# Performance work log

Hardware: AMD Instinct MI355X
Metric: run time of the kernel (lower is better)

## Reference

```python
import jax, jax.numpy as jnp
import numpy as np

IMG = 640.0  # square input image, strides 16/32 -> 40x40 and 20x20 grids

def _decode_level(raw, stride):
    # raw: [B, 5+C, H, W] -> [B, H*W, 5+C] with xy/wh decoded (get_output_and_grid)
    b, ch, h, w = raw.shape
    out = raw.transpose(0, 2, 3, 1).reshape(b, h * w, ch)
    yv, xv = jnp.meshgrid(jnp.arange(h), jnp.arange(w), indexing='ij')
    gx = xv.reshape(-1).astype(raw.dtype)
    gy = yv.reshape(-1).astype(raw.dtype)
    xy = (out[..., :2] + jnp.stack([gx, gy], -1)[None]) * stride
    wh = jnp.exp(out[..., 2:4]) * stride
    out = jnp.concatenate([xy, wh, out[..., 4:]], -1)
    return out, gx, gy, jnp.full((h * w,), stride, raw.dtype)

def _pairwise_iou(a, b):
    # a:[M,4], b:[A,4] in cxcywh -> [M,A] (bboxes_iou, xyxy=False)
    tl = jnp.maximum(a[:, None, :2] - a[:, None, 2:] * 0.5, b[None, :, :2] - b[None, :, 2:] * 0.5)
    br = jnp.minimum(a[:, None, :2] + a[:, None, 2:] * 0.5, b[None, :, :2] + b[None, :, 2:] * 0.5)
    inter = jnp.prod(br - tl, -1) * (tl < br).all(-1)
    area_a = a[:, 2] * a[:, 3]
    area_b = b[:, 2] * b[:, 3]
    return inter / (area_a[:, None] + area_b[None, :] - inter + 1e-16)

def _iou_loss(p, t):
    # YOLOX IOUloss (loss_type='iou'): 1 - iou^2, elementwise over [..., 4] cxcywh
    tl = jnp.maximum(p[..., :2] - p[..., 2:] * 0.5, t[..., :2] - t[..., 2:] * 0.5)
    br = jnp.minimum(p[..., :2] + p[..., 2:] * 0.5, t[..., :2] + t[..., 2:] * 0.5)
    inter = jnp.prod(br - tl, -1) * (tl < br).all(-1)
    iou = inter / (p[..., 2] * p[..., 3] + t[..., 2] * t[..., 3] - inter + 1e-16)
    return 1.0 - iou ** 2

def _bce_logits(x, t):
    # BCEWithLogitsLoss(reduction='none') = softplus(x) - x*t (stable)
    return jnp.logaddexp(0.0, x) - x * t

def _assign_one(bbox_p, cls_p, obj_p, gtb, gtc, gtv, ax, ay, st):
    # SimOTA assignment for one image (mask form of get_assignments, which is @no_grad).
    # bbox_p:[A,4] cls_p:[A,C] obj_p:[A] gtb:[M,4] px cxcywh, gtv:[M] valid mask.
    m = gtb.shape[0]
    axc = (ax + 0.5) * st
    ayc = (ay + 0.5) * st
    gl = gtb[:, 0] - 0.5 * gtb[:, 2]; gr = gtb[:, 0] + 0.5 * gtb[:, 2]
    gtp = gtb[:, 1] - 0.5 * gtb[:, 3]; gbt = gtb[:, 1] + 0.5 * gtb[:, 3]
    in_box = ((axc[None] > gl[:, None]) & (axc[None] < gr[:, None]) &
              (ayc[None] > gtp[:, None]) & (ayc[None] < gbt[:, None])) & gtv[:, None]
    r = 2.5  # center_radius
    in_ctr = ((axc[None] > gtb[:, 0:1] - r * st[None]) & (axc[None] < gtb[:, 0:1] + r * st[None]) &
              (ayc[None] > gtb[:, 1:2] - r * st[None]) & (ayc[None] < gtb[:, 1:2] + r * st[None])) & gtv[:, None]
    fg_cand = (in_box | in_ctr).any(0)          # candidate anchors (fg_mask pre-filter)
    in_both = in_box & in_ctr
    ious = _pairwise_iou(gtb, bbox_p)            # [M,A]
    p = jnp.sqrt(jax.nn.sigmoid(cls_p) * jax.nn.sigmoid(obj_p)[:, None])[None]  # [1,A,C]
    t = jax.nn.one_hot(gtc, cls_p.shape[-1], dtype=p.dtype)[:, None, :]          # [M,1,C]
    eps = 1e-12
    cls_cost = -(t * jnp.log(p + eps) + (1.0 - t) * jnp.log(1.0 - p + eps)).sum(-1)
    invalid = (~fg_cand)[None] | (~gtv)[:, None]
    cost = cls_cost - 3.0 * jnp.log(ious + 1e-8) + 1e5 * (~in_both) + 1e9 * invalid
    ious_m = jnp.where(invalid, 0.0, ious)
    topk, _ = jax.lax.top_k(ious_m, 10)
    dk = jnp.maximum(topk.sum(-1).astype(jnp.int32), 1)  # dynamic_k, clamp min=1
    dk = jnp.where(gtv, dk, 0)
    ranks = jnp.argsort(jnp.argsort(cost, axis=1), axis=1)
    matching = ranks < dk[:, None]                        # top dynamic_k lowest-cost anchors per gt
    conflict = matching.sum(0) > 1
    best_gt = jnp.argmin(cost, 0)
    matching = jnp.where(conflict[None], jnp.arange(m)[:, None] == best_gt[None], matching)
    fg = matching.any(0)
    matched = jnp.argmax(matching, 0).astype(jnp.int32)
    pred_iou = jnp.where(matching, ious, 0.0).sum(0)
    return fg, matched, pred_iou

def _forward(out_l0, out_l1, gt_boxes, gt_classes, num_gts):
    ncls = out_l0.shape[1] - 5
    decs, xs, ys, ss = [], [], [], []
    for raw, stride in ((out_l0, 16.0), (out_l1, 32.0)):
        d, gx, gy, s = _decode_level(raw, stride)
        decs.append(d); xs.append(gx); ys.append(gy); ss.append(s)
    outputs = jnp.concatenate(decs, 1)  # [B, A, 5+C]
    ax = jnp.concatenate(xs); ay = jnp.concatenate(ys); st = jnp.concatenate(ss)
    bbox_p = outputs[..., :4]; obj_p = outputs[..., 4]; cls_p = outputs[..., 5:]
    gtb = gt_boxes * IMG  # normalized -> pixels (imgs_w == imgs_h == IMG)
    gtv = jnp.arange(gt_boxes.shape[1])[None, :] < num_gts[:, None]
    sg = jax.lax.stop_gradient  # get_assignments runs under torch.no_grad
    fg, matched, pred_iou = jax.vmap(_assign_one, in_axes=(0, 0, 0, 0, 0, 0, None, None, None))(
        sg(bbox_p), sg(cls_p), sg(obj_p), sg(gtb), gt_classes, gtv, ax, ay, st)
    fgf = fg.astype(outputs.dtype)
    cls_t = jax.nn.one_hot(jnp.take_along_axis(gt_classes, matched, 1), ncls,
                           dtype=outputs.dtype) * pred_iou[..., None] * fgf[..., None]
    reg_t = jnp.take_along_axis(gtb, matched[..., None], 1)  # [B,A,4]
    num_fg = jnp.maximum(fgf.sum(), 1.0)
    loss_iou = (_iou_loss(bbox_p, reg_t) * fgf).sum() / num_fg
    loss_obj = _bce_logits(obj_p, fgf).sum() / num_fg
    loss_cls = (_bce_logits(cls_p, cls_t) * fgf[..., None]).sum() / num_fg
    total = 5.0 * loss_iou + loss_obj + loss_cls
    return (total, 5.0 * loss_iou, loss_obj, loss_cls,
            num_fg / jnp.maximum(num_gts.sum().astype(outputs.dtype), 1.0))

def setup_inputs() -> dict:
    key = jax.random.key(0)
    k1, k2, k3, k4, k5 = jax.random.split(key, 5)
    return {
        'out_l0': jax.random.normal(k1, (64, 25, 40, 40), jnp.float32),
        'out_l1': jax.random.normal(k2, (64, 25, 20, 20), jnp.float32),
        'gt_boxes': jax.random.uniform(k3, (64, 100, 4), jnp.float32, 1e-3, 1.0),
        'gt_classes': jax.random.randint(k4, (64, 100), 0, 20).astype(jnp.int32),
        'num_gts': jax.random.randint(k5, (64,), 0, 100).astype(jnp.int32),
    }

def reference(out_l0, out_l1, gt_boxes, gt_classes, num_gts):
    return _forward(out_l0, out_l1, gt_boxes, gt_classes, num_gts)
```

## Files before the change

### kernel.cpp

```cpp
#include <hip/hip_runtime.h>
#include <cfloat>
#include <climits>

#define NB 64
#define NA 2000
#define NAP 2048
#define NA0 1600
#define NC 20
#define NM 100

__device__ __forceinline__ void anchor_geom(int a, float& axc, float& ayc, float& st) {
    if (a < NA0) {
        st = 16.0f;
        int x = a % 40, y = a / 40;
        axc = ((float)x + 0.5f) * 16.0f;
        ayc = ((float)y + 0.5f) * 16.0f;
    } else {
        st = 32.0f;
        int aa = a - NA0;
        int x = aa % 20, y = aa / 20;
        axc = ((float)x + 0.5f) * 32.0f;
        ayc = ((float)y + 0.5f) * 32.0f;
    }
}

__device__ __forceinline__ float cost_pair(const float4 g, float clsc, const float4 pb,
                                           float axc, float ayc, float st, bool fc) {
    float tlx = fmaxf(g.x - 0.5f * g.z, pb.x - 0.5f * pb.z);
    float tly = fmaxf(g.y - 0.5f * g.w, pb.y - 0.5f * pb.w);
    float brx = fminf(g.x + 0.5f * g.z, pb.x + 0.5f * pb.z);
    float bry = fminf(g.y + 0.5f * g.w, pb.y + 0.5f * pb.w);
    float inter = (brx - tlx) * (bry - tly);
    bool ok = (tlx < brx) && (tly < bry);
    inter = ok ? inter : 0.0f;
    float iou = inter / ((g.z * g.w + pb.z * pb.w) - inter + 1e-16f);
    bool ib = (axc > g.x - 0.5f * g.z) && (axc < g.x + 0.5f * g.z)
           && (ayc > g.y - 0.5f * g.w) && (ayc < g.y + 0.5f * g.w);
    bool ic = (axc > g.x - 2.5f * st) && (axc < g.x + 2.5f * st)
           && (ayc > g.y - 2.5f * st) && (ayc < g.y + 2.5f * st);
    return ((clsc - 3.0f * __logf(iou + 1e-8f)) + ((ib && ic) ? 0.0f : 1e5f)) + (fc ? 0.0f : 1e9f);
}

__device__ __forceinline__ unsigned int wave_max_u32(unsigned int x) {
    unsigned int y;
    y = (unsigned)__builtin_amdgcn_update_dpp((int)x, (int)x, 0x111, 0xf, 0xf, false); x = max(x, y);
    y = (unsigned)__builtin_amdgcn_update_dpp((int)x, (int)x, 0x112, 0xf, 0xf, false); x = max(x, y);
    y = (unsigned)__builtin_amdgcn_update_dpp((int)x, (int)x, 0x114, 0xf, 0xf, false); x = max(x, y);
    y = (unsigned)__builtin_amdgcn_update_dpp((int)x, (int)x, 0x118, 0xf, 0xf, false); x = max(x, y);
    y = (unsigned)__builtin_amdgcn_update_dpp((int)x, (int)x, 0x142, 0xa, 0xf, false); x = max(x, y);
    y = (unsigned)__builtin_amdgcn_update_dpp((int)x, (int)x, 0x143, 0xc, 0xf, false); x = max(x, y);
    return (unsigned)__builtin_amdgcn_readlane((int)x, 63);
}
__device__ __forceinline__ unsigned int wave_min_u32(unsigned int x) {
    unsigned int y;
    y = (unsigned)__builtin_amdgcn_update_dpp((int)x, (int)x, 0x111, 0xf, 0xf, false); x = min(x, y);
    y = (unsigned)__builtin_amdgcn_update_dpp((int)x, (int)x, 0x112, 0xf, 0xf, false); x = min(x, y);
    y = (unsigned)__builtin_amdgcn_update_dpp((int)x, (int)x, 0x114, 0xf, 0xf, false); x = min(x, y);
    y = (unsigned)__builtin_amdgcn_update_dpp((int)x, (int)x, 0x118, 0xf, 0xf, false); x = min(x, y);
    y = (unsigned)__builtin_amdgcn_update_dpp((int)x, (int)x, 0x142, 0xa, 0xf, false); x = min(x, y);
    y = (unsigned)__builtin_amdgcn_update_dpp((int)x, (int)x, 0x143, 0xc, 0xf, false); x = min(x, y);
    return (unsigned)__builtin_amdgcn_readlane((int)x, 63);
}

__global__ __launch_bounds__(256) void k_decode(const float* __restrict__ l0, const float* __restrict__ l1,
                                                const float* __restrict__ gt_boxes, const int* __restrict__ num_gts,
                                                float4* __restrict__ dec, float* __restrict__ qq,
                                                unsigned long long* __restrict__ fgw, unsigned int* __restrict__ cm,
                                                float* __restrict__ sp) {
    int b = blockIdx.y;
    int a = blockIdx.x * 256 + threadIdx.x;
    int lane = threadIdx.x & 63;
    __shared__ float4 sext[NM];
    __shared__ float2 sctr[NM];
    __shared__ int sng;
    if (threadIdx.x < NM) {
        float4 g = ((const float4*)gt_boxes)[b * NM + threadIdx.x];
        g.x *= 640.0f; g.y *= 640.0f; g.z *= 640.0f; g.w *= 640.0f;
        sext[threadIdx.x] = make_float4(g.x - 0.5f * g.z, g.x + 0.5f * g.z,
                                        g.y - 0.5f * g.w, g.y + 0.5f * g.w);
        sctr[threadIdx.x] = make_float2(g.x, g.y);
    }
    if (threadIdx.x == 0) sng = num_gts[b];
    __syncthreads();

    bool real = a < NA;
    size_t pidx = (size_t)b * NAP + a;

    if (!real) {
        dec[pidx] = make_float4(0.f, 0.f, 0.f, 0.f);
#pragma unroll
        for (int c = 0; c < NC; c++) qq[((size_t)b * NC + c) * NAP + a] = 0.0f;
        cm[pidx] = 0;
        sp[pidx] = 0.0f;
        unsigned long long mk = __ballot(0);
        if (lane == 0) fgw[(size_t)b * 32 + (a >> 6)] = mk;
        return;
    }

    float v[25];
    if (a < NA0) {
        const float* p = l0 + (size_t)b * 25 * NA0 + a;
#pragma unroll
        for (int c = 0; c < 25; c++) v[c] = p[(size_t)c * NA0];
    } else {
        const float* p = l1 + (size_t)b * 25 * 400 + (a - NA0);
#pragma unroll
        for (int c = 0; c < 25; c++) v[c] = p[(size_t)c * 400];
    }
    float axc, ayc, st;
    anchor_geom(a, axc, ayc, st);
    float gx, gy;
    if (a < NA0) { gx = (float)(a % 40); gy = (float)(a / 40); }
    else { int aa = a - NA0; gx = (float)(aa % 20); gy = (float)(aa / 20); }
    float4 pb;
    pb.x = (v[0] + gx) * st;
    pb.y = (v[1] + gy) * st;
    pb.z = expf(v[2]) * st;
    pb.w = expf(v[3]) * st;
    dec[pidx] = pb;

    float sob = 1.0f / (1.0f + __expf(-v[4]));
    float d[NC];
    float s = 0.0f;
    float spv = 0.0f;
#pragma unroll
    for (int c = 0; c < NC; c++) {
        float x = v[5 + c];
        float sc = 1.0f / (1.0f + __expf(-x));
        float p = sqrtf(sc * sob);
        float lp = __logf(p + 1e-12f);
        float lq = __logf(1.0f - p + 1e-12f);
        s += -lq;
        d[c] = lq - lp;
        spv += fmaxf(x, 0.0f) + log1pf(__expf(-fabsf(x)));
    }
#pragma unroll
    for (int c = 0; c < NC; c++)
        qq[((size_t)b * NC + c) * NAP + a] = s + d[c];
    sp[pidx] = spv;

    int ng = sng;
    int f = 0;
    float rst = 2.5f * st;
    for (int m = 0; m < ng; m++) {
        float4 e = sext[m];
        float2 cc = sctr[m];
        bool ib = (axc > e.x) && (axc < e.y) && (ayc > e.z) && (ayc < e.w);
        bool ic = (axc > cc.x - rst) && (axc < cc.x + rst) && (ayc > cc.y - rst) && (ayc < cc.y + rst);
        if (ib || ic) { f = 1; break; }
    }
    unsigned long long mk = __ballot(f);
    if (lane == 0) fgw[(size_t)b * 32 + (a >> 6)] = mk;
    cm[pidx] = 0;
}

__global__ __launch_bounds__(256) void k_assign(const float* __restrict__ gt_boxes, const int* __restrict__ gt_classes,
                                                const int* __restrict__ num_gts, const float4* __restrict__ dec,
                                                const float* __restrict__ qq, const unsigned long long* __restrict__ fgw,
                                                unsigned int* __restrict__ cm) {
    int lane = threadIdx.x & 63;
    int wv = __builtin_amdgcn_readfirstlane((int)(threadIdx.x >> 6));
    int rloc = wv >> 1, half = wv & 1;
    int row = __builtin_amdgcn_readfirstlane((int)(blockIdx.x * 2 + rloc));
    int b = row / NM, m = row - b * NM;
    bool valid = (m < num_gts[b]);

    __shared__ unsigned int lA[2][2][10];
    __shared__ unsigned int lB[2][2][10];
    __shared__ unsigned int lmeta[2];
    __shared__ unsigned int lthr[2];

    unsigned int ik[16], ck[16];
    size_t bNA = (size_t)b * NAP;
    unsigned int inc = (1u << 20) + (unsigned)m;

    if (valid) {
        float4 g = ((const float4*)gt_boxes)[b * NM + m];
        g.x *= 640.0f; g.y *= 640.0f; g.z *= 640.0f; g.w *= 640.0f;
        int tc = gt_classes[b * NM + m];
        const float* qrow = qq + ((size_t)b * NC + tc) * NAP;

        float glx = g.x - 0.5f * g.z, grx = g.x + 0.5f * g.z;
        float gty = g.y - 0.5f * g.w, gby = g.y + 0.5f * g.w;
        float areag = g.z * g.w;
        float c16l = g.x - 40.0f, c16r = g.x + 40.0f, c16t = g.y - 40.0f, c16b = g.y + 40.0f;
        float c32l = g.x - 80.0f, c32r = g.x + 80.0f, c32t = g.y - 80.0f, c32b = g.y + 80.0f;

#pragma unroll
        for (int j = 0; j < 16; j++) {
            int jj = half * 16 + j;
            int a = jj * 64 + lane;
            bool lvl0 = jj < 25;
            float stj = lvl0 ? 16.0f : 32.0f;
            int rel = lvl0 ? a : (a - NA0);
            int W = lvl0 ? 40 : 20;
            int gyv = rel / W;
            int gxv = rel - gyv * W;
            float axc = ((float)gxv + 0.5f) * stj;
            float ayc = ((float)gyv + 0.5f) * stj;
            unsigned long long fw = fgw[(size_t)b * 32 + jj];
            bool fc = (fw >> lane) & 1ULL;
            float4 pb = dec[bNA + a];
            float clsc = qrow[a];
            float tlx = fmaxf(glx, pb.x - 0.5f * pb.z);
            float tly = fmaxf(gty, pb.y - 0.5f * pb.w);
            float brx = fminf(grx, pb.x + 0.5f * pb.z);
            float bry = fminf(gby, pb.y + 0.5f * pb.w);
            float inter = (brx - tlx) * (bry - tly);
            bool ok = (tlx < brx) && (tly < bry);
            inter = ok ? inter : 0.0f;
            float iou = inter / ((areag + pb.z * pb.w) - inter + 1e-16f);
            bool ib = (axc > glx) && (axc < grx) && (ayc > gty) && (ayc < gby);
            bool ic = lvl0 ? ((axc > c16l) && (axc < c16r) && (ayc > c16t) && (ayc < c16b))
                           : ((axc > c32l) && (axc < c32r) && (ayc > c32t) && (ayc < c32b));
            float cc = ((clsc - 3.0f * __logf(iou + 1e-8f)) + ((ib && ic) ? 0.0f : 1e5f)) + (fc ? 0.0f : 1e9f);
            float im = fc ? iou : 0.0f;
            ik[j] = (__float_as_uint(im) & 0xFFFFF800u) | (unsigned)a;
            ck[j] = (__float_as_uint(cc) & 0xFFFFF800u) | (unsigned)a;
        }

        int k = 0;
#pragma unroll 1
        for (; k < 10; ++k) {
            unsigned int t[8];
#pragma unroll
            for (int h = 0; h < 8; h++) t[h] = max(ik[2 * h], ik[2 * h + 1]);
#pragma unroll
            for (int w = 4; w >= 1; w >>= 1)
#pragma unroll
                for (int h = 0; h < w; h++) t[h] = max(t[h], t[h + w]);
            unsigned int mx = wave_max_u32(t[0]);
            if ((mx & 0xFFFFF800u) == 0u) break;
            if (lane == 0) lA[rloc][half][k] = mx;
#pragma unroll
            for (int j = 0; j < 16; j++) ik[j] = (ik[j] == mx) ? 0u : ik[j];
        }
#pragma unroll 1
        for (; k < 10; ++k) if (lane == 0) lA[rloc][half][k] = 0u;
    }
    __syncthreads();

    if (valid && half == 0 && lane == 0) {
        int i0 = 0, i1 = 0;
        float s = 0.0f;
        for (int k = 0; k < 10; k++) {
            unsigned int a0 = lA[rloc][0][i0], a1 = lA[rloc][1][i1];
            unsigned int mx;
            if (a1 > a0) { mx = a1; i1++; } else { mx = a0; i0++; }
            s += __uint_as_float(mx & 0xFFFFF800u);
        }
        int dk = (int)s;
        if (dk < 1) dk = 1;
        lmeta[rloc] = (unsigned)dk;
    }
    __syncthreads();

    int dkv = 0;
    if (valid) dkv = __builtin_amdgcn_readfirstlane((int)lmeta[rloc]);

    if (valid) {
#pragma unroll 1
        for (int k = 0; k < dkv; k++) {
            unsigned int t[8];
#pragma unroll
            for (int h = 0; h < 8; h++) t[h] = min(ck[2 * h], ck[2 * h + 1]);
#pragma unroll
            for (int w = 4; w >= 1; w >>= 1)
#pragma unroll
                for (int h = 0; h < w; h++) t[h] = min(t[h], t[h + w]);
            unsigned int mn = wave_min_u32(t[0]);
            if (lane == 0) lB[rloc][half][k] = mn;
#pragma unroll
            for (int j = 0; j < 16; j++) ck[j] = (ck[j] == mn) ? 0xFFFFFFFFu : ck[j];
        }
    }
    __syncthreads();

    if (valid && half == 0 && lane == 0) {
        int i0 = 0, i1 = 0;
        unsigned int thr = 0;
        for (int k = 0; k < dkv; k++) {
            unsigned int a0 = lB[rloc][0][i0], a1 = lB[rloc][1][i1];
            if (a1 < a0) { thr = a1; i1++; } else { thr = a0; i0++; }
        }
        lthr[rloc] = thr;
    }
    __syncthreads();

    if (valid) {
        unsigned int thr = (unsigned)__builtin_amdgcn_readfirstlane((int)lthr[rloc]);
        unsigned int mb = 0;
#pragma unroll
        for (int j = 0; j < 16; j++) if (ck[j] <= thr) mb |= 1u << j;
#pragma unroll 1
        for (int k = 0; k < dkv; k++) {
            unsigned int e = lB[rloc][half][k];
            if (e <= thr) {
                unsigned int idx = e & 0x7FFu;
                if ((int)(idx & 63u) == lane) mb |= 1u << ((int)(idx >> 6) - half * 16);
            }
        }
#pragma unroll
        for (int j = 0; j < 16; j++) {
            if ((mb >> j) & 1u) atomicAdd(&cm[bNA + (size_t)(half * 16 + j) * 64 + lane], inc);
        }
    }
}

__global__ __launch_bounds__(256) void k_conflict(const float* __restrict__ gt_boxes, const int* __restrict__ gt_classes,
                                                  const int* __restrict__ num_gts, const float4* __restrict__ dec,
                                                  const float* __restrict__ qq, const unsigned long long* __restrict__ fgw,
                                                  unsigned int* __restrict__ cm) {
    int gtid = blockIdx.x * 256 + threadIdx.x;
    int lane = threadIdx.x & 63;
    int base = gtid & ~63;
    unsigned int word = cm[gtid];
    unsigned long long msk = __ballot((word >> 20) >= 2u);
    if (msk == 0ull) return;
    int b = base >> 11;
    int ng = num_gts[b];
    while (msk) {
        int t = __ffsll((long long)msk) - 1;
        msk &= msk - 1;
        int idx = base + t;
        int a = idx & (NAP - 1);
        float4 pb = dec[idx];
        float axc, ayc, st;
        anchor_geom(a, axc, ayc, st);
        bool fc = (fgw[(size_t)b * 32 + (a >> 6)] >> (a & 63)) & 1ULL;
        unsigned int best = 0xFFFFFFFFu;
#pragma unroll
        for (int half = 0; half < 2; half++) {
            int m = half * 64 + lane;
            if (m < ng) {
                float4 g = ((const float4*)gt_boxes)[b * NM + m];
                g.x *= 640.0f; g.y *= 640.0f; g.z *= 640.0f; g.w *= 640.0f;
                int tcm = gt_classes[b * NM + m];
                float clsc = qq[((size_t)b * NC + tcm) * NAP + a];
                float cc = cost_pair(g, clsc, pb, axc, ayc, st, fc);
                unsigned int key = (__float_as_uint(cc) & 0xFFFFF800u) | (unsigned)m;
                best = min(best, key);
            }
        }
#pragma unroll
        for (int o = 1; o < 64; o <<= 1) {
            unsigned int ov = (unsigned int)__shfl_xor((int)best, o);
            best = min(best, ov);
        }
        if (lane == 0) cm[idx] = (1u << 20) | (best & 0x7FFu);
    }
}

__global__ __launch_bounds__(256) void k_resolve(const float* __restrict__ l0, const float* __restrict__ l1,
                                                 const float* __restrict__ gt_boxes, const int* __restrict__ gt_classes,
                                                 const float4* __restrict__ dec,
                                                 const unsigned int* __restrict__ cm,
                                                 const float* __restrict__ sp,
                                                 float* __restrict__ partials) {
    int idx = blockIdx.x * 256 + threadIdx.x;
    int b = idx / NA, a = idx - b * NA;
    size_t pidx = (size_t)b * NAP + a;

    float objv;
    if (a < NA0) objv = l0[((size_t)b * 25 + 4) * NA0 + a];
    else         objv = l1[((size_t)b * 25 + 4) * 400 + (a - NA0)];

    unsigned int word = cm[pidx];
    bool fg = (word >> 20) > 0;
    float fgf = fg ? 1.0f : 0.0f;
    float lobj = (fmaxf(objv, 0.0f) + log1pf(expf(-fabsf(objv)))) - objv * fgf;
    float liou = 0.0f, lcls = 0.0f;

    if (fg) {
        float4 pb = dec[pidx];
        int m = (int)(word & 0xFFFFFu);
        float4 g = ((const float4*)gt_boxes)[b * NM + m];
        g.x *= 640.0f; g.y *= 640.0f; g.z *= 640.0f; g.w *= 640.0f;
        float tlx = fmaxf(pb.x - 0.5f * pb.z, g.x - 0.5f * g.z);
        float tly = fmaxf(pb.y - 0.5f * pb.w, g.y - 0.5f * g.w);
        float brx = fminf(pb.x + 0.5f * pb.z, g.x + 0.5f * g.z);
        float bry = fminf(pb.y + 0.5f * pb.w, g.y + 0.5f * g.w);
        float inter = (brx - tlx) * (bry - tly);
        bool ok = (tlx < brx) && (tly < bry);
        inter = ok ? inter : 0.0f;
        float iou = inter / ((pb.z * pb.w + g.z * g.w) - inter + 1e-16f);
        liou = 1.0f - iou * iou;
        float piou = iou;
        int tcm = gt_classes[b * NM + m];
        float x_t;
        if (a < NA0) x_t = l0[((size_t)b * 25 + 5 + tcm) * NA0 + a];
        else         x_t = l1[((size_t)b * 25 + 5 + tcm) * 400 + (a - NA0)];
        lcls = sp[pidx] - x_t * piou;
    }

    __shared__ float s0[256], s1[256], s2[256], s3[256];
    int t = threadIdx.x;
    s0[t] = lobj; s1[t] = liou; s2[t] = lcls; s3[t] = fgf;
    __syncthreads();
    for (int o = 128; o > 0; o >>= 1) {
        if (t < o) { s0[t] += s0[t + o]; s1[t] += s1[t + o]; s2[t] += s2[t + o]; s3[t] += s3[t + o]; }
        __syncthreads();
    }
    if (t == 0) {
        partials[blockIdx.x * 4 + 0] = s0[0];
        partials[blockIdx.x * 4 + 1] = s1[0];
        partials[blockIdx.x * 4 + 2] = s2[0];
        partials[blockIdx.x * 4 + 3] = s3[0];
    }
}

__global__ __launch_bounds__(256) void k_final(const float* __restrict__ partials, int nblocks,
                                               const int* __restrict__ num_gts, float* __restrict__ out) {
    __shared__ float s0[256], s1[256], s2[256], s3[256];
    int t = threadIdx.x;
    float a0 = 0, a1 = 0, a2 = 0, a3 = 0;
    for (int i = t; i < nblocks; i += 256) {
        a0 += partials[i * 4 + 0];
        a1 += partials[i * 4 + 1];
        a2 += partials[i * 4 + 2];
        a3 += partials[i * 4 + 3];
    }
    s0[t] = a0; s1[t] = a1; s2[t] = a2; s3[t] = a3;
    __syncthreads();
    for (int o = 128; o > 0; o >>= 1) {
        if (t < o) { s0[t] += s0[t + o]; s1[t] += s1[t + o]; s2[t] += s2[t + o]; s3[t] += s3[t + o]; }
        __syncthreads();
    }
    if (t == 0) {
        int sg = 0;
        for (int i = 0; i < NB; i++) sg += num_gts[i];
        float num_fg = fmaxf(s3[0], 1.0f);
        float li5 = 5.0f * (s1[0] / num_fg);
        float lo = s0[0] / num_fg;
        float lcx = s2[0] / num_fg;
        out[0] = li5 + lo + lcx;
        out[1] = li5;
        out[2] = lo;
        out[3] = lcx;
        out[4] = num_fg / fmaxf((float)sg, 1.0f);
    }
}

extern "C" void kernel_launch(void* const* d_in, const int* in_sizes, int n_in,
                              void* d_out, int out_size, void* d_ws, size_t ws_size,
                              hipStream_t stream) {
    const float* l0 = (const float*)d_in[0];
    const float* l1 = (const float*)d_in[1];
    const float* gt_boxes = (const float*)d_in[2];
    const int* gt_classes = (const int*)d_in[3];
    const int* num_gts = (const int*)d_in[4];
    float* out = (float*)d_out;

    char* w = (char*)d_ws;
    float4* dec = (float4*)(w);
    float* qq   = (float*)(w + 2097152);
    unsigned long long* fgw = (unsigned long long*)(w + 12582912);
    unsigned int* cm = (unsigned int*)(w + 12599296);
    float* sp   = (float*)(w + 13123584);
    float* partials = (float*)(w + 13647872);

    (void)n_in; (void)in_sizes; (void)out_size; (void)ws_size;

    k_decode<<<dim3(8, NB), 256, 0, stream>>>(l0, l1, gt_boxes, num_gts, dec, qq, fgw, cm, sp);
    k_assign<<<(NB * NM) / 2, 256, 0, stream>>>(gt_boxes, gt_classes, num_gts, dec, qq, fgw, cm);
    k_conflict<<<(NB * NAP) / 256, 256, 0, stream>>>(gt_boxes, gt_classes, num_gts, dec, qq, fgw, cm);
    k_resolve<<<(NB * NA) / 256, 256, 0, stream>>>(l0, l1, gt_boxes, gt_classes, dec, cm, sp, partials);
    k_final<<<1, 256, 0, stream>>>(partials, (NB * NA) / 256, num_gts, out);
}
```

Baseline: 73.57 us.

## Fuse conflict resolution into loss kernel and precompute predicted box extents

Merges the conflict-resolution kernel into the loss/reduction kernel, which now iterates over padded anchor indices and resolves multi-GT anchors in registers before computing the losses. Decoded boxes are stored as precomputed edge extents plus an area instead of center/size, which removes repeated half-width arithmetic in the per-pair cost loop. Padding anchors no longer write zeros to the intermediate buffers. The cost is a larger resolve kernel with divergent work and an extra area buffer. Skipping the padding writes depends on every consumer ignoring those slots.

```diff
diff --git a/kernel.cpp b/kernel.cpp
--- a/kernel.cpp
+++ b/kernel.cpp
@@ -24,18 +24,19 @@
     }
 }
 
-__device__ __forceinline__ float cost_pair(const float4 g, float clsc, const float4 pb,
-                                           float axc, float ayc, float st, bool fc) {
-    float tlx = fmaxf(g.x - 0.5f * g.z, pb.x - 0.5f * pb.z);
-    float tly = fmaxf(g.y - 0.5f * g.w, pb.y - 0.5f * pb.w);
-    float brx = fminf(g.x + 0.5f * g.z, pb.x + 0.5f * pb.z);
-    float bry = fminf(g.y + 0.5f * g.w, pb.y + 0.5f * pb.w);
+__device__ __forceinline__ float cost_row(const float4 g, float clsc, const float4 pe, float areaP,
+                                          float axc, float ayc, float st, bool fc) {
+    float glx = g.x - 0.5f * g.z, grx = g.x + 0.5f * g.z;
+    float gty = g.y - 0.5f * g.w, gby = g.y + 0.5f * g.w;
+    float tlx = fmaxf(glx, pe.x);
+    float tly = fmaxf(gty, pe.z);
+    float brx = fminf(grx, pe.y);
+    float bry = fminf(gby, pe.w);
     float inter = (brx - tlx) * (bry - tly);
     bool ok = (tlx < brx) && (tly < bry);
     inter = ok ? inter : 0.0f;
-    float iou = inter / ((g.z * g.w + pb.z * pb.w) - inter + 1e-16f);
-    bool ib = (axc > g.x - 0.5f * g.z) && (axc < g.x + 0.5f * g.z)
-           && (ayc > g.y - 0.5f * g.w) && (ayc < g.y + 0.5f * g.w);
+    float iou = inter / ((g.z * g.w + areaP) - inter + 1e-16f);
+    bool ib = (axc > glx) && (axc < grx) && (ayc > gty) && (ayc < gby);
     bool ic = (axc > g.x - 2.5f * st) && (axc < g.x + 2.5f * st)
            && (ayc > g.y - 2.5f * st) && (ayc < g.y + 2.5f * st);
     return ((clsc - 3.0f * __logf(iou + 1e-8f)) + ((ib && ic) ? 0.0f : 1e5f)) + (fc ? 0.0f : 1e9f);
@@ -64,7 +65,8 @@
 
 __global__ __launch_bounds__(256) void k_decode(const float* __restrict__ l0, const float* __restrict__ l1,
                                                 const float* __restrict__ gt_boxes, const int* __restrict__ num_gts,
-                                                float4* __restrict__ dec, float* __restrict__ qq,
+                                                float4* __restrict__ ext, float* __restrict__ decA,
+                                                float* __restrict__ qq,
                                                 unsigned long long* __restrict__ fgw, unsigned int* __restrict__ cm,
                                                 float* __restrict__ sp) {
     int b = blockIdx.y;
@@ -83,17 +85,9 @@
     if (threadIdx.x == 0) sng = num_gts[b];
     __syncthreads();
 
-    bool real = a < NA;
     size_t pidx = (size_t)b * NAP + a;
-
-    if (!real) {
-        dec[pidx] = make_float4(0.f, 0.f, 0.f, 0.f);
-#pragma unroll
-        for (int c = 0; c < NC; c++) qq[((size_t)b * NC + c) * NAP + a] = 0.0f;
+    if (a >= NA) {
         cm[pidx] = 0;
-        sp[pidx] = 0.0f;
-        unsigned long long mk = __ballot(0);
-        if (lane == 0) fgw[(size_t)b * 32 + (a >> 6)] = mk;
         return;
     }
 
@@ -117,7 +111,9 @@
     pb.y = (v[1] + gy) * st;
     pb.z = expf(v[2]) * st;
     pb.w = expf(v[3]) * st;
-    dec[pidx] = pb;
+    ext[pidx] = make_float4(pb.x - 0.5f * pb.z, pb.x + 0.5f * pb.z,
+                            pb.y - 0.5f * pb.w, pb.y + 0.5f * pb.w);
+    decA[pidx] = pb.z * pb.w;
 
     float sob = 1.0f / (1.0f + __expf(-v[4]));
     float d[NC];
@@ -155,7 +151,8 @@
 }
 
 __global__ __launch_bounds__(256) void k_assign(const float* __restrict__ gt_boxes, const int* __restrict__ gt_classes,
-                                                const int* __restrict__ num_gts, const float4* __restrict__ dec,
+                                                const int* __restrict__ num_gts, const float4* __restrict__ ext,
+                                                const float* __restrict__ decA,
                                                 const float* __restrict__ qq, const unsigned long long* __restrict__ fgw,
                                                 unsigned int* __restrict__ cm) {
     int lane = threadIdx.x & 63;
@@ -200,16 +197,17 @@
             float ayc = ((float)gyv + 0.5f) * stj;
             unsigned long long fw = fgw[(size_t)b * 32 + jj];
             bool fc = (fw >> lane) & 1ULL;
-            float4 pb = dec[bNA + a];
+            float4 pe = ext[bNA + a];
+            float areaP = decA[bNA + a];
             float clsc = qrow[a];
-            float tlx = fmaxf(glx, pb.x - 0.5f * pb.z);
-            float tly = fmaxf(gty, pb.y - 0.5f * pb.w);
-            float brx = fminf(grx, pb.x + 0.5f * pb.z);
-            float bry = fminf(gby, pb.y + 0.5f * pb.w);
+            float tlx = fmaxf(glx, pe.x);
+            float tly = fmaxf(gty, pe.z);
+            float brx = fminf(grx, pe.y);
+            float bry = fminf(gby, pe.w);
             float inter = (brx - tlx) * (bry - tly);
             bool ok = (tlx < brx) && (tly < bry);
             inter = ok ? inter : 0.0f;
-            float iou = inter / ((areag + pb.z * pb.w) - inter + 1e-16f);
+            float iou = inter / ((areag + areaP) - inter + 1e-16f);
             bool ib = (axc > glx) && (axc < grx) && (ayc > gty) && (ayc < gby);
             bool ic = lvl0 ? ((axc > c16l) && (axc < c16r) && (ayc > c16t) && (ayc < c16b))
                            : ((axc > c32l) && (axc < c32r) && (ayc > c32t) && (ayc < c32b));
@@ -307,90 +305,90 @@
     }
 }
 
-__global__ __launch_bounds__(256) void k_conflict(const float* __restrict__ gt_boxes, const int* __restrict__ gt_classes,
-                                                  const int* __restrict__ num_gts, const float4* __restrict__ dec,
-                                                  const float* __restrict__ qq, const unsigned long long* __restrict__ fgw,
-                                                  unsigned int* __restrict__ cm) {
-    int gtid = blockIdx.x * 256 + threadIdx.x;
-    int lane = threadIdx.x & 63;
-    int base = gtid & ~63;
-    unsigned int word = cm[gtid];
-    unsigned long long msk = __ballot((word >> 20) >= 2u);
-    if (msk == 0ull) return;
-    int b = base >> 11;
-    int ng = num_gts[b];
-    while (msk) {
-        int t = __ffsll((long long)msk) - 1;
-        msk &= msk - 1;
-        int idx = base + t;
-        int a = idx & (NAP - 1);
-        float4 pb = dec[idx];
-        float axc, ayc, st;
-        anchor_geom(a, axc, ayc, st);
-        bool fc = (fgw[(size_t)b * 32 + (a >> 6)] >> (a & 63)) & 1ULL;
-        unsigned int best = 0xFFFFFFFFu;
-#pragma unroll
-        for (int half = 0; half < 2; half++) {
-            int m = half * 64 + lane;
-            if (m < ng) {
-                float4 g = ((const float4*)gt_boxes)[b * NM + m];
-                g.x *= 640.0f; g.y *= 640.0f; g.z *= 640.0f; g.w *= 640.0f;
-                int tcm = gt_classes[b * NM + m];
-                float clsc = qq[((size_t)b * NC + tcm) * NAP + a];
-                float cc = cost_pair(g, clsc, pb, axc, ayc, st, fc);
-                unsigned int key = (__float_as_uint(cc) & 0xFFFFF800u) | (unsigned)m;
-                best = min(best, key);
-            }
-        }
-#pragma unroll
-        for (int o = 1; o < 64; o <<= 1) {
-            unsigned int ov = (unsigned int)__shfl_xor((int)best, o);
-            best = min(best, ov);
-        }
-        if (lane == 0) cm[idx] = (1u << 20) | (best & 0x7FFu);
-    }
-}
-
 __global__ __launch_bounds__(256) void k_resolve(const float* __restrict__ l0, const float* __restrict__ l1,
                                                  const float* __restrict__ gt_boxes, const int* __restrict__ gt_classes,
-                                                 const float4* __restrict__ dec,
+                                                 const int* __restrict__ num_gts,
+                                                 const float4* __restrict__ ext, const float* __restrict__ decA,
+                                                 const float* __restrict__ qq, const unsigned long long* __restrict__ fgw,
                                                  const unsigned int* __restrict__ cm,
                                                  const float* __restrict__ sp,
                                                  float* __restrict__ partials) {
-    int idx = blockIdx.x * 256 + threadIdx.x;
-    int b = idx / NA, a = idx - b * NA;
-    size_t pidx = (size_t)b * NAP + a;
-
-    float objv;
-    if (a < NA0) objv = l0[((size_t)b * 25 + 4) * NA0 + a];
-    else         objv = l1[((size_t)b * 25 + 4) * 400 + (a - NA0)];
-
-    unsigned int word = cm[pidx];
-    bool fg = (word >> 20) > 0;
-    float fgf = fg ? 1.0f : 0.0f;
-    float lobj = (fmaxf(objv, 0.0f) + log1pf(expf(-fabsf(objv)))) - objv * fgf;
-    float liou = 0.0f, lcls = 0.0f;
-
-    if (fg) {
-        float4 pb = dec[pidx];
-        int m = (int)(word & 0xFFFFFu);
-        float4 g = ((const float4*)gt_boxes)[b * NM + m];
-        g.x *= 640.0f; g.y *= 640.0f; g.z *= 640.0f; g.w *= 640.0f;
-        float tlx = fmaxf(pb.x - 0.5f * pb.z, g.x - 0.5f * g.z);
-        float tly = fmaxf(pb.y - 0.5f * pb.w, g.y - 0.5f * g.w);
-        float brx = fminf(pb.x + 0.5f * pb.z, g.x + 0.5f * g.z);
-        float bry = fminf(pb.y + 0.5f * pb.w, g.y + 0.5f * g.w);
-        float inter = (brx - tlx) * (bry - tly);
-        bool ok = (tlx < brx) && (tly < bry);
-        inter = ok ? inter : 0.0f;
-        float iou = inter / ((pb.z * pb.w + g.z * g.w) - inter + 1e-16f);
-        liou = 1.0f - iou * iou;
-        float piou = iou;
-        int tcm = gt_classes[b * NM + m];
-        float x_t;
-        if (a < NA0) x_t = l0[((size_t)b * 25 + 5 + tcm) * NA0 + a];
-        else         x_t = l1[((size_t)b * 25 + 5 + tcm) * 400 + (a - NA0)];
-        lcls = sp[pidx] - x_t * piou;
+    int gtid = blockIdx.x * 256 + threadIdx.x;
+    int lane = threadIdx.x & 63;
+    int b = gtid >> 11;
+    int a = gtid & (NAP - 1);
+    bool real = a < NA;
+
+    unsigned int word = real ? cm[gtid] : 0u;
+    int mres = (int)(word & 0xFFFFFu);
+
+    unsigned long long msk = __ballot((word >> 20) >= 2u);
+    if (msk != 0ull) {
+        int base = gtid & ~63;
+        int ng = num_gts[b];
+        while (msk) {
+            int t = __ffsll((long long)msk) - 1;
+            msk &= msk - 1;
+            int idx = base + t;
+            int aa = idx & (NAP - 1);
+            float4 pe = ext[idx];
+            float areaP = decA[idx];
+            float axc, ayc, st;
+            anchor_geom(aa, axc, ayc, st);
+            bool fcq = (fgw[(size_t)b * 32 + (aa >> 6)] >> (aa & 63)) & 1ULL;
+            unsigned int best = 0xFFFFFFFFu;
+#pragma unroll
+            for (int half = 0; half < 2; half++) {
+                int m = half * 64 + lane;
+                if (m < ng) {
+                    float4 g = ((const float4*)gt_boxes)[b * NM + m];
+                    g.x *= 640.0f; g.y *= 640.0f; g.z *= 640.0f; g.w *= 640.0f;
+                    int tcm = gt_classes[b * NM + m];
+                    float clsc = qq[((size_t)b * NC + tcm) * NAP + aa];
+                    float cc = cost_row(g, clsc, pe, areaP, axc, ayc, st, fcq);
+                    unsigned int key = (__float_as_uint(cc) & 0xFFFFF800u) | (unsigned)m;
+                    best = min(best, key);
+                }
+            }
+#pragma unroll
+            for (int o = 1; o < 64; o <<= 1) {
+                unsigned int ov = (unsigned int)__shfl_xor((int)best, o);
+                best = min(best, ov);
+            }
+            if (lane == t) mres = (int)(best & 0x7FFu);
+        }
+    }
+
+    float lobj = 0.0f, liou = 0.0f, lcls = 0.0f, fgf = 0.0f;
+    if (real) {
+        float objv;
+        if (a < NA0) objv = l0[((size_t)b * 25 + 4) * NA0 + a];
+        else         objv = l1[((size_t)b * 25 + 4) * 400 + (a - NA0)];
+        bool fg = (word >> 20) > 0;
+        fgf = fg ? 1.0f : 0.0f;
+        lobj = (fmaxf(objv, 0.0f) + log1pf(expf(-fabsf(objv)))) - objv * fgf;
+        if (fg) {
+            float4 pe = ext[gtid];
+            float areaP = decA[gtid];
+            int m = mres;
+            float4 g = ((const float4*)gt_boxes)[b * NM + m];
+            g.x *= 640.0f; g.y *= 640.0f; g.z *= 640.0f; g.w *= 640.0f;
+            float tlx = fmaxf(pe.x, g.x - 0.5f * g.z);
+            float tly = fmaxf(pe.z, g.y - 0.5f * g.w);
+            float brx = fminf(pe.y, g.x + 0.5f * g.z);
+            float bry = fminf(pe.w, g.y + 0.5f * g.w);
+            float inter = (brx - tlx) * (bry - tly);
+            bool ok = (tlx < brx) && (tly < bry);
+            inter = ok ? inter : 0.0f;
+            float iou = inter / ((areaP + g.z * g.w) - inter + 1e-16f);
+            liou = 1.0f - iou * iou;
+            float piou = iou;
+            int tcm = gt_classes[b * NM + m];
+            float x_t;
+            if (a < NA0) x_t = l0[((size_t)b * 25 + 5 + tcm) * NA0 + a];
+            else         x_t = l1[((size_t)b * 25 + 5 + tcm) * 400 + (a - NA0)];
+            lcls = sp[gtid] - x_t * piou;
+        }
     }
 
     __shared__ float s0[256], s1[256], s2[256], s3[256];
@@ -452,18 +450,18 @@
     float* out = (float*)d_out;
 
     char* w = (char*)d_ws;
-    float4* dec = (float4*)(w);
-    float* qq   = (float*)(w + 2097152);
-    unsigned long long* fgw = (unsigned long long*)(w + 12582912);
-    unsigned int* cm = (unsigned int*)(w + 12599296);
-    float* sp   = (float*)(w + 13123584);
-    float* partials = (float*)(w + 13647872);
+    float4* ext  = (float4*)(w);
+    float* decA  = (float*)(w + 2097152);
+    float* qq    = (float*)(w + 2621440);
+    unsigned long long* fgw = (unsigned long long*)(w + 13107200);
+    unsigned int* cm = (unsigned int*)(w + 13123584);
+    float* sp    = (float*)(w + 13647872);
+    float* partials = (float*)(w + 14172160);
 
     (void)n_in; (void)in_sizes; (void)out_size; (void)ws_size;
 
-    k_decode<<<dim3(8, NB), 256, 0, stream>>>(l0, l1, gt_boxes, num_gts, dec, qq, fgw, cm, sp);
-    k_assign<<<(NB * NM) / 2, 256, 0, stream>>>(gt_boxes, gt_classes, num_gts, dec, qq, fgw, cm);
-    k_conflict<<<(NB * NAP) / 256, 256, 0, stream>>>(gt_boxes, gt_classes, num_gts, dec, qq, fgw, cm);
-    k_resolve<<<(NB * NA) / 256, 256, 0, stream>>>(l0, l1, gt_boxes, gt_classes, dec, cm, sp, partials);
-    k_final<<<1, 256, 0, stream>>>(partials, (NB * NA) / 256, num_gts, out);
-}
+    k_decode<<<dim3(8, NB), 256, 0, stream>>>(l0, l1, gt_boxes, num_gts, ext, decA, qq, fgw, cm, sp);
+    k_assign<<<(NB * NM) / 2, 256, 0, stream>>>(gt_boxes, gt_classes, num_gts, ext, decA, qq, fgw, cm);
+    k_resolve<<<(NB * NAP) / 256, 256, 0, stream>>>(l0, l1, gt_boxes, gt_classes, num_gts, ext, decA, qq, fgw, cm, sp, partials);
+    k_final<<<1, 256, 0, stream>>>(partials, (NB * NAP) / 256, num_gts, out);
+}
```

Result: no change. 73.02 us, median of 2 (-0.8%).
